# Performance work log

Measured on AMD Instinct MI355X. Metric: run time of the kernel, lower is better.

The kernel has to match this reference:

```python
import jax, jax.numpy as jnp
import numpy as np

D_MODEL, JOINT_DIM, VOCAB = 512, 640, 1024
B, T, U = 4, 256, 64


def setup_inputs() -> dict:
    key = jax.random.key(0)
    ks = jax.random.split(key, 8)
    s_in = 1.0 / np.sqrt(D_MODEL)
    s_j = 1.0 / np.sqrt(JOINT_DIM)
    return {
        "enc": jax.random.normal(ks[0], (B, T, D_MODEL), jnp.float32),
        "pred": jax.random.normal(ks[1], (B, U, D_MODEL), jnp.float32),
        "enc_w": jax.random.uniform(ks[2], (JOINT_DIM, D_MODEL), jnp.float32, -s_in, s_in),
        "enc_b": jax.random.uniform(ks[3], (JOINT_DIM,), jnp.float32, -s_in, s_in),
        "pred_w": jax.random.uniform(ks[4], (JOINT_DIM, D_MODEL), jnp.float32, -s_in, s_in),
        "pred_b": jax.random.uniform(ks[5], (JOINT_DIM,), jnp.float32, -s_in, s_in),
        "out_w": jax.random.uniform(ks[6], (VOCAB, JOINT_DIM), jnp.float32, -s_j, s_j),
        "out_b": jax.random.uniform(ks[7], (VOCAB,), jnp.float32, -s_j, s_j),
    }


def reference(enc, pred, enc_w, enc_b, pred_w, pred_b, out_w, out_b):
    # project encoder (B,T,J) and predictor (B,U,J)
    e = jnp.einsum("btd,jd->btj", enc, enc_w) + enc_b
    p = jnp.einsum("bud,jd->buj", pred, pred_w) + pred_b
    # broadcast add over the (T,U) grid, tanh, then vocab projection
    z = jnp.tanh(e[:, :, None, :] + p[:, None, :, :])  # (B,T,U,J)
    logits = jnp.einsum("btuj,vj->btuv", z, out_w) + out_b  # (B,T,U,V)
    return logits
```

## Files before the change

### kernel.cpp

```cpp
#include <hip/hip_runtime.h>
#include <cstdint>
#include <cstddef>


typedef __attribute__((ext_vector_type(8))) __bf16 bf16x8;
typedef __attribute__((ext_vector_type(4))) float f32x4;

__device__ __forceinline__ int swz64(int row, int kElem) {
  return (row << 6) + (kElem ^ ((row & 7) << 3));
}
__device__ __forceinline__ int swz32(int row, int kElem) {
  return (row << 5) + ((kElem & 7) | (((kElem >> 3) ^ ((row >> 2) & 3)) << 3));
}

__device__ __forceinline__ float fast_tanh(float x) {
  float e = __builtin_amdgcn_exp2f(x * 2.88539008177793f);
  return 1.0f - 2.0f * __builtin_amdgcn_rcpf(e + 1.0f);
}

__device__ __forceinline__ void gload_lds16(const void* g, void* l) {
  __builtin_amdgcn_global_load_lds(
      (const __attribute__((address_space(1))) void*)g,
      (__attribute__((address_space(3))) void*)l, 16, 0, 0);
}

__device__ void proj_tile(const float* __restrict__ A, const float* __restrict__ W,
                          const float* __restrict__ bias, __bf16* __restrict__ C,
                          int mt, int nt, __bf16* As, __bf16* Bs)
{
  const int tid  = threadIdx.x;
  const int r = tid & 127, half = tid >> 7;
  const int lane = tid & 63, wv = tid >> 6;
  const int wm = wv >> 1, wn = wv & 1;

  const float* arow = A + (size_t)(mt * 128 + r) * 512 + half * 32;
  const float* wrow = W + (size_t)(nt * 128 + r) * 512 + half * 32;

  f32x4 acc[4][4] = {};

  for (int k0 = 0; k0 < 512; k0 += 64) {
#pragma unroll
    for (int s = 0; s < 4; ++s) {
      f32x4 a0 = *(const f32x4*)(arow + k0 + s * 8);
      f32x4 a1 = *(const f32x4*)(arow + k0 + s * 8 + 4);
      f32x4 w0 = *(const f32x4*)(wrow + k0 + s * 8);
      f32x4 w1 = *(const f32x4*)(wrow + k0 + s * 8 + 4);
      bf16x8 za, zw;
#pragma unroll
      for (int j = 0; j < 4; ++j) {
        za[j] = (__bf16)a0[j]; za[4 + j] = (__bf16)a1[j];
        zw[j] = (__bf16)w0[j]; zw[4 + j] = (__bf16)w1[j];
      }
      const int kk = half * 32 + s * 8;
      *(bf16x8*)&As[swz64(r, kk)] = za;
      *(bf16x8*)&Bs[swz64(r, kk)] = zw;
    }
    __syncthreads();
#pragma unroll
    for (int kk = 0; kk < 2; ++kk) {
      bf16x8 af[4], bfr[4];
#pragma unroll
      for (int i = 0; i < 4; ++i) {
        af[i]  = *(const bf16x8*)&As[swz64(wm * 64 + i * 16 + (lane & 15), kk * 32 + (lane >> 4) * 8)];
        bfr[i] = *(const bf16x8*)&Bs[swz64(wn * 64 + i * 16 + (lane & 15), kk * 32 + (lane >> 4) * 8)];
      }
#pragma unroll
      for (int mi = 0; mi < 4; ++mi)
#pragma unroll
        for (int ni = 0; ni < 4; ++ni)
          acc[mi][ni] = __builtin_amdgcn_mfma_f32_16x16x32_bf16(af[mi], bfr[ni], acc[mi][ni], 0, 0, 0);
    }
    __syncthreads();
  }

  const int rowbase = mt * 128 + wm * 64;
  const int colbase = nt * 128 + wn * 64;
#pragma unroll
  for (int ni = 0; ni < 4; ++ni) {
    const int col = colbase + ni * 16 + (lane & 15);
    const float bb = bias[col];
#pragma unroll
    for (int mi = 0; mi < 4; ++mi) {
      const int row = rowbase + mi * 16 + (lane >> 4) * 4;
#pragma unroll
      for (int rg = 0; rg < 4; ++rg)
        C[(size_t)(row + rg) * 640 + col] = (__bf16)(acc[mi][ni][rg] + bb);
    }
  }
}

__global__ __launch_bounds__(256) void prep_kernel(
    const float* __restrict__ enc,  const float* __restrict__ enc_w,  const float* __restrict__ enc_b,
    const float* __restrict__ pred, const float* __restrict__ pred_w, const float* __restrict__ pred_b,
    const float* __restrict__ out_w,
    __bf16* __restrict__ E, __bf16* __restrict__ P, __bf16* __restrict__ Wb, int zpath)
{
  __shared__ __align__(16) __bf16 As[128 * 64];
  __shared__ __align__(16) __bf16 Bs[128 * 64];
  const int bid = blockIdx.x;
  if (bid < 40) {
    proj_tile(enc, enc_w, enc_b, E, bid / 5, bid % 5, As, Bs);
  } else if (bid < 50) {
    proj_tile(pred, pred_w, pred_b, P, (bid - 40) / 5, (bid - 40) % 5, As, Bs);
  } else {
    const int gid = (bid - 50) * 256 + threadIdx.x;
    const int v  = gid / 80;
    const int j8 = gid % 80;
    f32x4 w0 = *(const f32x4*)(out_w + (size_t)v * 640 + j8 * 8);
    f32x4 w1 = *(const f32x4*)(out_w + (size_t)v * 640 + j8 * 8 + 4);
    bf16x8 z;
#pragma unroll
    for (int j = 0; j < 4; ++j) { z[j] = (__bf16)w0[j]; z[4 + j] = (__bf16)w1[j]; }
    if (zpath) {
      const int nb = v >> 8, rr = v & 255;
      const int kt = j8 >> 2;
      *(bf16x8*)(Wb + ((size_t)(nb * 20 + kt) << 13) + swz32(rr, (j8 & 3) * 8)) = z;
    } else {
      const int nb = v >> 7, rr = v & 127;
      const int kb = j8 >> 3, kk = (j8 & 7) * 8;
      *(bf16x8*)(Wb + ((size_t)(nb * 10 + kb) << 13) + swz64(rr, kk)) = z;
    }
  }
}

__global__ __launch_bounds__(256) void zprod_kernel(
    const __bf16* __restrict__ E, const __bf16* __restrict__ P,
    __bf16* __restrict__ Z)
{
  const int bid = blockIdx.x;
  const int mt = bid / 20, kt = bid % 20;
  const int row0 = mt << 8;
  const int b  = row0 >> 14;
  const int t0 = (row0 >> 6) & 255;
  __bf16* zdst = Z + ((size_t)bid << 13);

#pragma unroll
  for (int c = 0; c < 4; ++c) {
    const int o = c * 2048 + threadIdx.x * 8;
    const int r = o >> 5;
    const int cc = (o >> 3) & 3;
    const int k = kt * 32 + ((cc ^ ((r >> 2) & 3)) << 3);
    const __bf16* ep = E + (size_t)((b << 8) + t0 + (r >> 6)) * 640 + k;
    const __bf16* pp = P + (size_t)((b << 6) + (r & 63)) * 640 + k;
    bf16x8 e8 = *(const bf16x8*)ep;
    bf16x8 p8 = *(const bf16x8*)pp;
    bf16x8 z;
#pragma unroll
    for (int j = 0; j < 8; ++j)
      z[j] = (__bf16)fast_tanh((float)e8[j] + (float)p8[j]);
    *(bf16x8*)&zdst[o] = z;
  }
}

__global__ __launch_bounds__(512, 2) void joiner_ring(
    const __bf16* __restrict__ Z, const __bf16* __restrict__ Wb,
    const float* __restrict__ outb, float* __restrict__ out)
{
  __shared__ __align__(16) __bf16 As[4][8192];
  __shared__ __align__(16) __bf16 Bs[4][8192];
  const int wg = blockIdx.x;
  const int bid = (wg & 7) * 128 + (wg >> 3);
  const int mt = bid >> 2, nt = bid & 3;
  const int tid = threadIdx.x;
  const int lane = tid & 63, wv = tid >> 6;
  const int wm = wv >> 2, wn = wv & 3;

  const __bf16* zsrc = Z  + ((size_t)(mt * 20) << 13);
  const __bf16* wsrc = Wb + ((size_t)(nt * 20) << 13);

  f32x4 acc[8][4] = {};

  const int arow_s = ((wm * 128 + (lane & 15)) >> 2) & 3;
  const int brow_s = ((wn * 64  + (lane & 15)) >> 2) & 3;
  const int aoff = (wm * 128 + (lane & 15)) * 32 + (((lane >> 4) ^ arow_s) << 3);
  const int boff = (wn * 64  + (lane & 15)) * 32 + (((lane >> 4) ^ brow_s) << 3);

  auto stage = [&](int t) {
    const int s = t & 3;
    const size_t g = (size_t)t << 13;
#pragma unroll
    for (int c = 0; c < 2; ++c) {
      const int off = c * 4096 + wv * 512;
      gload_lds16(zsrc + g + off + lane * 8, &As[s][off]);
      gload_lds16(wsrc + g + off + lane * 8, &Bs[s][off]);
    }
  };

  stage(0); stage(1); stage(2);
  asm volatile("s_waitcnt vmcnt(8)" ::: "memory");
  __builtin_amdgcn_s_barrier();

#pragma unroll
  for (int t = 0; t < 20; ++t) {
    const int s = t & 3;
    if (t < 17) stage(t + 3);
    __builtin_amdgcn_s_setprio(1);
    bf16x8 bfr[4];
#pragma unroll
    for (int ni = 0; ni < 4; ++ni)
      bfr[ni] = *(const bf16x8*)&Bs[s][boff + ni * 512];
#pragma unroll
    for (int mi = 0; mi < 8; ++mi) {
      bf16x8 af = *(const bf16x8*)&As[s][aoff + mi * 512];
#pragma unroll
      for (int ni = 0; ni < 4; ++ni)
        acc[mi][ni] = __builtin_amdgcn_mfma_f32_16x16x32_bf16(af, bfr[ni], acc[mi][ni], 0, 0, 0);
    }
    __builtin_amdgcn_s_setprio(0);
    if (t < 19) {
      if (t < 17)       asm volatile("s_waitcnt vmcnt(8)" ::: "memory");
      else if (t == 17) asm volatile("s_waitcnt vmcnt(4)" ::: "memory");
      else              asm volatile("s_waitcnt vmcnt(0)" ::: "memory");
      __builtin_amdgcn_s_barrier();
    }
  }

  const int rowbase = (mt << 8) + wm * 128;
  const int colbase = (nt << 8) + wn * 64;
#pragma unroll
  for (int ni = 0; ni < 4; ++ni) {
    const int col = colbase + ni * 16 + (lane & 15);
    const float bb = outb[col];
#pragma unroll
    for (int mi = 0; mi < 8; ++mi) {
      const int row = rowbase + mi * 16 + (lane >> 4) * 4;
#pragma unroll
      for (int rg = 0; rg < 4; ++rg)
        out[(size_t)(row + rg) * 1024 + col] = acc[mi][ni][rg] + bb;
    }
  }
}

__global__ __launch_bounds__(512, 4) void joiner_fused(
    const __bf16* __restrict__ E, const __bf16* __restrict__ P,
    const __bf16* __restrict__ Wb, const float* __restrict__ outb,
    float* __restrict__ out)
{
  __shared__ __align__(16) __bf16 As[8192];
  __shared__ __align__(16) __bf16 Bs[2][16384];
  const int tid = threadIdx.x;
  const int nt = blockIdx.x & 3;
  const int mt = blockIdx.x >> 2;
  const int row0 = mt << 7;
  const int b  = row0 >> 14;
  const int t0 = (row0 >> 6) & 255;
  const int ar = tid & 127, h = tid >> 7;
  const int lane = tid & 63, wv = tid >> 6;
  const int wm = wv >> 2, wn = wv & 3;

  const __bf16* ep = E + (size_t)((b << 8) + t0 + (ar >> 6)) * 640 + h * 16;
  const __bf16* pp = P + (size_t)((b << 6) + (ar & 63)) * 640 + h * 16;

  f32x4 acc[4][4] = {};
  bf16x8 eA[2], pA[2];

  auto stageB2 = [&](int kt, __bf16* dst) {
#pragma unroll
    for (int c = 0; c < 4; ++c) {
      const int blk = nt * 2 + (c >> 1);
      const int inoff = (c & 1) * 4096 + wv * 512;
      gload_lds16(Wb + ((size_t)(blk * 10 + kt) << 13) + inoff + lane * 8,
                  dst + (c >> 1) * 8192 + inoff);
    }
  };
  auto loadEP = [&](int k0) {
#pragma unroll
    for (int c = 0; c < 2; ++c) {
      eA[c] = *(const bf16x8*)(ep + k0 + c * 8);
      pA[c] = *(const bf16x8*)(pp + k0 + c * 8);
    }
  };
  auto writeA = [&]() {
#pragma unroll
    for (int c = 0; c < 2; ++c) {
      bf16x8 z;
#pragma unroll
      for (int j = 0; j < 8; ++j)
        z[j] = (__bf16)fast_tanh((float)eA[c][j] + (float)pA[c][j]);
      *(bf16x8*)&As[swz64(ar, h * 16 + c * 8)] = z;
    }
  };
  auto compute = [&](const __bf16* Bsc) {
#pragma unroll
    for (int kk = 0; kk < 2; ++kk) {
      bf16x8 af[4], bfr[4];
#pragma unroll
      for (int i = 0; i < 4; ++i) {
        af[i]  = *(const bf16x8*)&As[swz64(wm * 64 + i * 16 + (lane & 15), kk * 32 + (lane >> 4) * 8)];
        bfr[i] = *(const bf16x8*)&Bsc[swz64(wn * 64 + i * 16 + (lane & 15), kk * 32 + (lane >> 4) * 8)];
      }
      asm volatile("s_waitcnt lgkmcnt(0)" ::: "memory");
      __builtin_amdgcn_sched_barrier(0);
      __builtin_amdgcn_s_setprio(1);
#pragma unroll
      for (int mi = 0; mi < 4; ++mi)
#pragma unroll
        for (int ni = 0; ni < 4; ++ni)
          acc[mi][ni] = __builtin_amdgcn_mfma_f32_16x16x32_bf16(af[mi], bfr[ni], acc[mi][ni], 0, 0, 0);
      __builtin_amdgcn_s_setprio(0);
    }
  };

  stageB2(0, Bs[0]);
  loadEP(0);
  writeA();
  asm volatile("s_waitcnt vmcnt(0) lgkmcnt(0)" ::: "memory");
  __builtin_amdgcn_s_barrier();

  for (int kt = 0; kt < 9; ++kt) {
    const int cur = kt & 1;
    stageB2(kt + 1, Bs[cur ^ 1]);
    loadEP((kt + 1) << 6);
    compute(Bs[cur]);
    __builtin_amdgcn_s_barrier();
    __builtin_amdgcn_sched_barrier(0);
    writeA();
    asm volatile("s_waitcnt lgkmcnt(0)" ::: "memory");
    __builtin_amdgcn_s_barrier();
  }
  compute(Bs[1]);

  const int rowbase = row0 + wm * 64;
  const int colbase = (nt << 8) + wn * 64;
#pragma unroll
  for (int ni = 0; ni < 4; ++ni) {
    const int col = colbase + ni * 16 + (lane & 15);
    const float bb = outb[col];
#pragma unroll
    for (int mi = 0; mi < 4; ++mi) {
      const int row = rowbase + mi * 16 + (lane >> 4) * 4;
#pragma unroll
      for (int rg = 0; rg < 4; ++rg)
        out[(size_t)(row + rg) * 1024 + col] = acc[mi][ni][rg] + bb;
    }
  }
}

extern "C" void kernel_launch(void* const* d_in, const int* in_sizes, int n_in,
                              void* d_out, int out_size, void* d_ws, size_t ws_size,
                              hipStream_t stream) {
  const float* enc    = (const float*)d_in[0];
  const float* pred   = (const float*)d_in[1];
  const float* enc_w  = (const float*)d_in[2];
  const float* enc_b  = (const float*)d_in[3];
  const float* pred_w = (const float*)d_in[4];
  const float* pred_b = (const float*)d_in[5];
  const float* out_w  = (const float*)d_in[6];
  const float* out_b  = (const float*)d_in[7];
  float* out = (float*)d_out;

  char* ws = (char*)d_ws;
  __bf16* E  = (__bf16*)(ws);
  __bf16* P  = (__bf16*)(ws + 1310720);
  __bf16* Wb = (__bf16*)(ws + 1638400);
  __bf16* Z  = (__bf16*)(ws + 2949120);

  const int zpath = (ws_size >= (size_t)86835200) ? 1 : 0;

  prep_kernel<<<dim3(370), dim3(256), 0, stream>>>(
      enc, enc_w, enc_b, pred, pred_w, pred_b, out_w, E, P, Wb, zpath);

  if (zpath) {
    zprod_kernel<<<dim3(5120), dim3(256), 0, stream>>>(E, P, Z);
    joiner_ring<<<dim3(1024), dim3(512), 0, stream>>>(Z, Wb, out_b, out);
  } else {
    joiner_fused<<<dim3(2048), dim3(512), 0, stream>>>(E, P, Wb, out_b, out);
  }
}
```

Measured before the change: 173.2 us.

## Restructure joiner GEMM into 8-phase half-tile pipeline with 64-wide K tiles

```diff
diff --git a/kernel.cpp b/kernel.cpp
--- a/kernel.cpp
+++ b/kernel.cpp
@@ -8,9 +8,6 @@
 
 __device__ __forceinline__ int swz64(int row, int kElem) {
   return (row << 6) + (kElem ^ ((row & 7) << 3));
-}
-__device__ __forceinline__ int swz32(int row, int kElem) {
-  return (row << 5) + ((kElem & 7) | (((kElem >> 3) ^ ((row >> 2) & 3)) << 3));
 }
 
 __device__ __forceinline__ float fast_tanh(float x) {
@@ -112,9 +109,10 @@
 #pragma unroll
     for (int j = 0; j < 4; ++j) { z[j] = (__bf16)w0[j]; z[4 + j] = (__bf16)w1[j]; }
     if (zpath) {
-      const int nb = v >> 8, rr = v & 255;
-      const int kt = j8 >> 2;
-      *(bf16x8*)(Wb + ((size_t)(nb * 20 + kt) << 13) + swz32(rr, (j8 & 3) * 8)) = z;
+      const int nt = v >> 8, vv = v & 255;
+      const int half = vv >> 7, rr = vv & 127;
+      const int kt = j8 >> 3, kk = (j8 & 7) * 8;
+      *(bf16x8*)(Wb + (((size_t)(nt * 10 + kt) * 2 + half) << 13) + swz64(rr, kk)) = z;
     } else {
       const int nb = v >> 7, rr = v & 127;
       const int kb = j8 >> 3, kk = (j8 & 7) * 8;
@@ -128,20 +126,19 @@
     __bf16* __restrict__ Z)
 {
   const int bid = blockIdx.x;
-  const int mt = bid / 20, kt = bid % 20;
-  const int row0 = mt << 8;
-  const int b  = row0 >> 14;
-  const int t0 = (row0 >> 6) & 255;
-  __bf16* zdst = Z + ((size_t)bid << 13);
-
-#pragma unroll
-  for (int c = 0; c < 4; ++c) {
+  const int mt = bid / 10, kt = bid % 10;
+  __bf16* zdst = Z + ((size_t)bid << 14);
+
+#pragma unroll
+  for (int c = 0; c < 8; ++c) {
     const int o = c * 2048 + threadIdx.x * 8;
-    const int r = o >> 5;
-    const int cc = (o >> 3) & 3;
-    const int k = kt * 32 + ((cc ^ ((r >> 2) & 3)) << 3);
-    const __bf16* ep = E + (size_t)((b << 8) + t0 + (r >> 6)) * 640 + k;
-    const __bf16* pp = P + (size_t)((b << 6) + (r & 63)) * 640 + k;
+    const int half = o >> 13, oo = o & 8191;
+    const int rr = oo >> 6;
+    const int r = half * 128 + rr;
+    const int k = kt * 64 + ((oo & 63) ^ ((rr & 7) << 3));
+    const int grow = mt * 256 + r;
+    const __bf16* ep = E + (size_t)(grow >> 6) * 640 + k;
+    const __bf16* pp = P + (size_t)(((grow >> 14) << 6) | (grow & 63)) * 640 + k;
     bf16x8 e8 = *(const bf16x8*)ep;
     bf16x8 p8 = *(const bf16x8*)pp;
     bf16x8 z;
@@ -152,12 +149,12 @@
   }
 }
 
-__global__ __launch_bounds__(512, 2) void joiner_ring(
+__global__ __launch_bounds__(512, 2) void joiner_8p(
     const __bf16* __restrict__ Z, const __bf16* __restrict__ Wb,
     const float* __restrict__ outb, float* __restrict__ out)
 {
-  __shared__ __align__(16) __bf16 As[4][8192];
-  __shared__ __align__(16) __bf16 Bs[4][8192];
+  __shared__ __align__(16) __bf16 As[2][2][8192];
+  __shared__ __align__(16) __bf16 Bs[2][2][8192];
   const int wg = blockIdx.x;
   const int bid = (wg & 7) * 128 + (wg >> 3);
   const int mt = bid >> 2, nt = bid & 3;
@@ -165,68 +162,133 @@
   const int lane = tid & 63, wv = tid >> 6;
   const int wm = wv >> 2, wn = wv & 3;
 
+  const int rb  = wm * 16 + (lane & 15);
+  const int cb  = wn * 16 + (lane & 15);
+  const int kb8 = (lane >> 4) * 8;
+
   const __bf16* zsrc = Z  + ((size_t)(mt * 20) << 13);
   const __bf16* wsrc = Wb + ((size_t)(nt * 20) << 13);
 
   f32x4 acc[8][4] = {};
 
-  const int arow_s = ((wm * 128 + (lane & 15)) >> 2) & 3;
-  const int brow_s = ((wn * 64  + (lane & 15)) >> 2) & 3;
-  const int aoff = (wm * 128 + (lane & 15)) * 32 + (((lane >> 4) ^ arow_s) << 3);
-  const int boff = (wn * 64  + (lane & 15)) * 32 + (((lane >> 4) ^ brow_s) << 3);
-
-  auto stage = [&](int t) {
-    const int s = t & 3;
-    const size_t g = (size_t)t << 13;
-#pragma unroll
-    for (int c = 0; c < 2; ++c) {
-      const int off = c * 4096 + wv * 512;
-      gload_lds16(zsrc + g + off + lane * 8, &As[s][off]);
-      gload_lds16(wsrc + g + off + lane * 8, &Bs[s][off]);
-    }
-  };
-
-  stage(0); stage(1); stage(2);
-  asm volatile("s_waitcnt vmcnt(8)" ::: "memory");
+  auto stA = [&](int kt, int half) {
+    __bf16* dst = &As[kt & 1][half][wv * 512];
+    const __bf16* src = zsrc + (((size_t)kt * 2 + half) << 13) + wv * 512 + lane * 8;
+    gload_lds16(src, dst);
+    gload_lds16(src + 4096, dst + 4096);
+  };
+  auto stB = [&](int kt, int half) {
+    __bf16* dst = &Bs[kt & 1][half][wv * 512];
+    const __bf16* src = wsrc + (((size_t)kt * 2 + half) << 13) + wv * 512 + lane * 8;
+    gload_lds16(src, dst);
+    gload_lds16(src + 4096, dst + 4096);
+  };
+
+  stA(0, 0); stB(0, 0); stB(0, 1); stA(0, 1);
+  stA(1, 0); stB(1, 0); stB(1, 1);
+  asm volatile("s_waitcnt vmcnt(6)" ::: "memory");
   __builtin_amdgcn_s_barrier();
 
 #pragma unroll
-  for (int t = 0; t < 20; ++t) {
-    const int s = t & 3;
-    if (t < 17) stage(t + 3);
+  for (int k = 0; k < 10; ++k) {
+    const int d = k & 1;
+    const __bf16* A0 = &As[d][0][0];
+    const __bf16* A1 = &As[d][1][0];
+    const __bf16* B0 = &Bs[d][0][0];
+    const __bf16* B1 = &Bs[d][1][0];
+    bf16x8 afl[4][2], afh[4][2], bl[2][2], bh[2][2];
+
+#pragma unroll
+    for (int f = 0; f < 4; ++f)
+#pragma unroll
+      for (int kk = 0; kk < 2; ++kk)
+        afl[f][kk] = *(const bf16x8*)&A0[swz64(f * 32 + rb, kk * 32 + kb8)];
+#pragma unroll
+    for (int g = 0; g < 2; ++g)
+#pragma unroll
+      for (int kk = 0; kk < 2; ++kk)
+        bl[g][kk] = *(const bf16x8*)&B0[swz64(g * 64 + cb, kk * 32 + kb8)];
+    if (k < 9) stA(k + 1, 1);
+    if (k == 9) asm volatile("s_waitcnt vmcnt(0)" ::: "memory");
+    else        asm volatile("s_waitcnt vmcnt(6)" ::: "memory");
+    __builtin_amdgcn_s_barrier();
+    asm volatile("s_waitcnt lgkmcnt(0)" ::: "memory");
+    __builtin_amdgcn_sched_barrier(0);
     __builtin_amdgcn_s_setprio(1);
-    bf16x8 bfr[4];
-#pragma unroll
-    for (int ni = 0; ni < 4; ++ni)
-      bfr[ni] = *(const bf16x8*)&Bs[s][boff + ni * 512];
-#pragma unroll
-    for (int mi = 0; mi < 8; ++mi) {
-      bf16x8 af = *(const bf16x8*)&As[s][aoff + mi * 512];
-#pragma unroll
-      for (int ni = 0; ni < 4; ++ni)
-        acc[mi][ni] = __builtin_amdgcn_mfma_f32_16x16x32_bf16(af, bfr[ni], acc[mi][ni], 0, 0, 0);
-    }
+#pragma unroll
+    for (int kk = 0; kk < 2; ++kk)
+#pragma unroll
+      for (int f = 0; f < 4; ++f)
+#pragma unroll
+        for (int g = 0; g < 2; ++g)
+          acc[f][g] = __builtin_amdgcn_mfma_f32_16x16x32_bf16(afl[f][kk], bl[g][kk], acc[f][g], 0, 0, 0);
     __builtin_amdgcn_s_setprio(0);
-    if (t < 19) {
-      if (t < 17)       asm volatile("s_waitcnt vmcnt(8)" ::: "memory");
-      else if (t == 17) asm volatile("s_waitcnt vmcnt(4)" ::: "memory");
-      else              asm volatile("s_waitcnt vmcnt(0)" ::: "memory");
-      __builtin_amdgcn_s_barrier();
-    }
-  }
-
-  const int rowbase = (mt << 8) + wm * 128;
-  const int colbase = (nt << 8) + wn * 64;
-#pragma unroll
-  for (int ni = 0; ni < 4; ++ni) {
-    const int col = colbase + ni * 16 + (lane & 15);
+    __builtin_amdgcn_s_barrier();
+
+#pragma unroll
+    for (int g = 0; g < 2; ++g)
+#pragma unroll
+      for (int kk = 0; kk < 2; ++kk)
+        bh[g][kk] = *(const bf16x8*)&B1[swz64(g * 64 + cb, kk * 32 + kb8)];
+    if (k < 8) stA(k + 2, 0);
+    __builtin_amdgcn_s_barrier();
+    asm volatile("s_waitcnt lgkmcnt(0)" ::: "memory");
+    __builtin_amdgcn_sched_barrier(0);
+    __builtin_amdgcn_s_setprio(1);
+#pragma unroll
+    for (int kk = 0; kk < 2; ++kk)
+#pragma unroll
+      for (int f = 0; f < 4; ++f)
+#pragma unroll
+        for (int g = 0; g < 2; ++g)
+          acc[f][2 + g] = __builtin_amdgcn_mfma_f32_16x16x32_bf16(afl[f][kk], bh[g][kk], acc[f][2 + g], 0, 0, 0);
+    __builtin_amdgcn_s_setprio(0);
+    __builtin_amdgcn_s_barrier();
+
+#pragma unroll
+    for (int f = 0; f < 4; ++f)
+#pragma unroll
+      for (int kk = 0; kk < 2; ++kk)
+        afh[f][kk] = *(const bf16x8*)&A1[swz64(f * 32 + rb, kk * 32 + kb8)];
+    if (k < 8) stB(k + 2, 0);
+    __builtin_amdgcn_s_barrier();
+    asm volatile("s_waitcnt lgkmcnt(0)" ::: "memory");
+    __builtin_amdgcn_sched_barrier(0);
+    __builtin_amdgcn_s_setprio(1);
+#pragma unroll
+    for (int kk = 0; kk < 2; ++kk)
+#pragma unroll
+      for (int f = 0; f < 4; ++f)
+#pragma unroll
+        for (int g = 0; g < 2; ++g)
+          acc[4 + f][2 + g] = __builtin_amdgcn_mfma_f32_16x16x32_bf16(afh[f][kk], bh[g][kk], acc[4 + f][2 + g], 0, 0, 0);
+    __builtin_amdgcn_s_setprio(0);
+    __builtin_amdgcn_s_barrier();
+
+    if (k < 8) stB(k + 2, 1);
+    __builtin_amdgcn_s_setprio(1);
+#pragma unroll
+    for (int kk = 0; kk < 2; ++kk)
+#pragma unroll
+      for (int f = 0; f < 4; ++f)
+#pragma unroll
+        for (int g = 0; g < 2; ++g)
+          acc[4 + f][g] = __builtin_amdgcn_mfma_f32_16x16x32_bf16(afh[f][kk], bl[g][kk], acc[4 + f][g], 0, 0, 0);
+    __builtin_amdgcn_s_setprio(0);
+  }
+
+  const int rowbase = (mt << 8) + wm * 16 + (lane >> 4) * 4;
+  const int colbase = (nt << 8) + wn * 16 + (lane & 15);
+#pragma unroll
+  for (int g = 0; g < 4; ++g) {
+    const int col = colbase + g * 64;
     const float bb = outb[col];
 #pragma unroll
-    for (int mi = 0; mi < 8; ++mi) {
-      const int row = rowbase + mi * 16 + (lane >> 4) * 4;
+    for (int f = 0; f < 8; ++f) {
+      const int row = rowbase + f * 32;
 #pragma unroll
       for (int rg = 0; rg < 4; ++rg)
-        out[(size_t)(row + rg) * 1024 + col] = acc[mi][ni][rg] + bb;
+        out[(size_t)(row + rg) * 1024 + col] = acc[f][g][rg] + bb;
     }
   }
 }
@@ -361,8 +423,8 @@
       enc, enc_w, enc_b, pred, pred_w, pred_b, out_w, E, P, Wb, zpath);
 
   if (zpath) {
-    zprod_kernel<<<dim3(5120), dim3(256), 0, stream>>>(E, P, Z);
-    joiner_ring<<<dim3(1024), dim3(512), 0, stream>>>(Z, Wb, out_b, out);
+    zprod_kernel<<<dim3(2560), dim3(256), 0, stream>>>(E, P, Z);
+    joiner_8p<<<dim3(1024), dim3(512), 0, stream>>>(Z, Wb, out_b, out);
   } else {
     joiner_fused<<<dim3(2048), dim3(512), 0, stream>>>(E, P, Wb, out_b, out);
   }
```

After: 154.5 us. 1.12x faster.

## Shrink joiner GEMM tile to 128x256 with double buffering and higher occupancy

Applied to the files above, without the earlier changes.

```diff
diff --git a/kernel.cpp b/kernel.cpp
--- a/kernel.cpp
+++ b/kernel.cpp
@@ -10,7 +10,7 @@
   return (row << 6) + (kElem ^ ((row & 7) << 3));
 }
 __device__ __forceinline__ int swz32(int row, int kElem) {
-  return (row << 5) + ((kElem & 7) | (((kElem >> 3) ^ ((row >> 2) & 3)) << 3));
+  return (row << 5) + ((kElem & 7) | (((kElem >> 3) ^ (row & 3)) << 3));
 }
 
 __device__ __forceinline__ float fast_tanh(float x) {
@@ -112,9 +112,12 @@
 #pragma unroll
     for (int j = 0; j < 4; ++j) { z[j] = (__bf16)w0[j]; z[4 + j] = (__bf16)w1[j]; }
     if (zpath) {
-      const int nb = v >> 8, rr = v & 255;
+      const int nt = v >> 8;
+      const int half = (v >> 7) & 1;
+      const int rr = v & 127;
       const int kt = j8 >> 2;
-      *(bf16x8*)(Wb + ((size_t)(nb * 20 + kt) << 13) + swz32(rr, (j8 & 3) * 8)) = z;
+      const int kk = (j8 & 3) * 8;
+      *(bf16x8*)(Wb + (((size_t)(nt * 20 + kt) * 2 + half) << 12) + swz32(rr, kk)) = z;
     } else {
       const int nb = v >> 7, rr = v & 127;
       const int kb = j8 >> 3, kk = (j8 & 7) * 8;
@@ -129,19 +132,17 @@
 {
   const int bid = blockIdx.x;
   const int mt = bid / 20, kt = bid % 20;
-  const int row0 = mt << 8;
-  const int b  = row0 >> 14;
-  const int t0 = (row0 >> 6) & 255;
-  __bf16* zdst = Z + ((size_t)bid << 13);
-
-#pragma unroll
-  for (int c = 0; c < 4; ++c) {
+  __bf16* zdst = Z + ((size_t)bid << 12);
+
+#pragma unroll
+  for (int c = 0; c < 2; ++c) {
     const int o = c * 2048 + threadIdx.x * 8;
     const int r = o >> 5;
     const int cc = (o >> 3) & 3;
-    const int k = kt * 32 + ((cc ^ ((r >> 2) & 3)) << 3);
-    const __bf16* ep = E + (size_t)((b << 8) + t0 + (r >> 6)) * 640 + k;
-    const __bf16* pp = P + (size_t)((b << 6) + (r & 63)) * 640 + k;
+    const int k = kt * 32 + ((cc ^ (r & 3)) << 3);
+    const int grow = mt * 128 + r;
+    const __bf16* ep = E + (size_t)(grow >> 6) * 640 + k;
+    const __bf16* pp = P + (size_t)(((grow >> 14) << 6) | (grow & 63)) * 640 + k;
     bf16x8 e8 = *(const bf16x8*)ep;
     bf16x8 p8 = *(const bf16x8*)pp;
     bf16x8 z;
@@ -152,77 +153,73 @@
   }
 }
 
-__global__ __launch_bounds__(512, 2) void joiner_ring(
+__global__ __launch_bounds__(512, 4) void joiner_2ph(
     const __bf16* __restrict__ Z, const __bf16* __restrict__ Wb,
     const float* __restrict__ outb, float* __restrict__ out)
 {
-  __shared__ __align__(16) __bf16 As[4][8192];
-  __shared__ __align__(16) __bf16 Bs[4][8192];
+  __shared__ __align__(16) __bf16 As[2][4096];
+  __shared__ __align__(16) __bf16 Bs[2][8192];
   const int wg = blockIdx.x;
-  const int bid = (wg & 7) * 128 + (wg >> 3);
+  const int bid = (wg & 7) * 256 + (wg >> 3);
   const int mt = bid >> 2, nt = bid & 3;
   const int tid = threadIdx.x;
   const int lane = tid & 63, wv = tid >> 6;
   const int wm = wv >> 2, wn = wv & 3;
-
-  const __bf16* zsrc = Z  + ((size_t)(mt * 20) << 13);
-  const __bf16* wsrc = Wb + ((size_t)(nt * 20) << 13);
-
-  f32x4 acc[8][4] = {};
-
-  const int arow_s = ((wm * 128 + (lane & 15)) >> 2) & 3;
-  const int brow_s = ((wn * 64  + (lane & 15)) >> 2) & 3;
-  const int aoff = (wm * 128 + (lane & 15)) * 32 + (((lane >> 4) ^ arow_s) << 3);
-  const int boff = (wn * 64  + (lane & 15)) * 32 + (((lane >> 4) ^ brow_s) << 3);
-
-  auto stage = [&](int t) {
-    const int s = t & 3;
-    const size_t g = (size_t)t << 13;
-#pragma unroll
-    for (int c = 0; c < 2; ++c) {
-      const int off = c * 4096 + wv * 512;
-      gload_lds16(zsrc + g + off + lane * 8, &As[s][off]);
-      gload_lds16(wsrc + g + off + lane * 8, &Bs[s][off]);
-    }
-  };
-
-  stage(0); stage(1); stage(2);
-  asm volatile("s_waitcnt vmcnt(8)" ::: "memory");
+  const int q = lane & 15;
+  const int chunk = (((lane >> 4) ^ (q & 3)) << 3);
+
+  const __bf16* zsrc = Z  + (size_t)mt * 81920;
+  const __bf16* wsrc = Wb + (size_t)nt * 163840;
+
+  const int abase = (wm * 64 + q) * 32 + chunk;
+  const int bbase = (wn * 64 + q) * 32 + chunk;
+
+  f32x4 acc[4][4] = {};
+
+  auto stage = [&](int k) {
+    const int d = k & 1;
+    const int wo = wv * 512;
+    gload_lds16(zsrc + k * 4096 + wo + lane * 8, &As[d][wo]);
+    gload_lds16(wsrc + k * 8192 + wo + lane * 8, &Bs[d][wo]);
+    gload_lds16(wsrc + k * 8192 + 4096 + wo + lane * 8, &Bs[d][4096 + wo]);
+  };
+
+  stage(0);
+  asm volatile("s_waitcnt vmcnt(0)" ::: "memory");
   __builtin_amdgcn_s_barrier();
 
-#pragma unroll
-  for (int t = 0; t < 20; ++t) {
-    const int s = t & 3;
-    if (t < 17) stage(t + 3);
+#pragma unroll 2
+  for (int k = 0; k < 20; ++k) {
+    const int d = k & 1;
+    if (k < 19) stage(k + 1);
+    bf16x8 af[4], bfr[4];
+#pragma unroll
+    for (int mi = 0; mi < 4; ++mi)
+      af[mi] = *(const bf16x8*)&As[d][abase + mi * 512];
+#pragma unroll
+    for (int ni = 0; ni < 4; ++ni)
+      bfr[ni] = *(const bf16x8*)&Bs[d][bbase + ni * 512];
     __builtin_amdgcn_s_setprio(1);
-    bf16x8 bfr[4];
-#pragma unroll
-    for (int ni = 0; ni < 4; ++ni)
-      bfr[ni] = *(const bf16x8*)&Bs[s][boff + ni * 512];
-#pragma unroll
-    for (int mi = 0; mi < 8; ++mi) {
-      bf16x8 af = *(const bf16x8*)&As[s][aoff + mi * 512];
+#pragma unroll
+    for (int mi = 0; mi < 4; ++mi)
 #pragma unroll
       for (int ni = 0; ni < 4; ++ni)
-        acc[mi][ni] = __builtin_amdgcn_mfma_f32_16x16x32_bf16(af, bfr[ni], acc[mi][ni], 0, 0, 0);
-    }
+        acc[mi][ni] = __builtin_amdgcn_mfma_f32_16x16x32_bf16(af[mi], bfr[ni], acc[mi][ni], 0, 0, 0);
     __builtin_amdgcn_s_setprio(0);
-    if (t < 19) {
-      if (t < 17)       asm volatile("s_waitcnt vmcnt(8)" ::: "memory");
-      else if (t == 17) asm volatile("s_waitcnt vmcnt(4)" ::: "memory");
-      else              asm volatile("s_waitcnt vmcnt(0)" ::: "memory");
+    if (k < 19) {
+      asm volatile("s_waitcnt vmcnt(0)" ::: "memory");
       __builtin_amdgcn_s_barrier();
     }
   }
 
-  const int rowbase = (mt << 8) + wm * 128;
+  const int rowbase = (mt << 7) + wm * 64;
   const int colbase = (nt << 8) + wn * 64;
 #pragma unroll
   for (int ni = 0; ni < 4; ++ni) {
-    const int col = colbase + ni * 16 + (lane & 15);
+    const int col = colbase + ni * 16 + q;
     const float bb = outb[col];
 #pragma unroll
-    for (int mi = 0; mi < 8; ++mi) {
+    for (int mi = 0; mi < 4; ++mi) {
       const int row = rowbase + mi * 16 + (lane >> 4) * 4;
 #pragma unroll
       for (int rg = 0; rg < 4; ++rg)
@@ -361,8 +358,8 @@
       enc, enc_w, enc_b, pred, pred_w, pred_b, out_w, E, P, Wb, zpath);
 
   if (zpath) {
-    zprod_kernel<<<dim3(5120), dim3(256), 0, stream>>>(E, P, Z);
-    joiner_ring<<<dim3(1024), dim3(512), 0, stream>>>(Z, Wb, out_b, out);
+    zprod_kernel<<<dim3(10240), dim3(256), 0, stream>>>(E, P, Z);
+    joiner_2ph<<<dim3(2048), dim3(512), 0, stream>>>(Z, Wb, out_b, out);
   } else {
     joiner_fused<<<dim3(2048), dim3(512), 0, stream>>>(E, P, Wb, out_b, out);
   }
```

Measured after the change: 163.0 us. 5.9% less time.
